# Kernel tuning notes

Hardware: AMD Instinct MI355X
Metric: run time of the kernel (lower is better)

The kernel has to match this reference:

```python
import math
import jax, jax.numpy as jnp
import numpy as np

# ---- static configuration (matches init_kwargs) ----
BATCH, F_IN, F_OUT = 8, 64, 128
B_IN, B_OUT = 32, 16
NL = B_OUT                    # spherical degrees l = 0..NL-1
MDIM = 2 * NL - 1             # dense order axis, m in [-(NL-1), NL-1]
N_BETA_G, N_ALPHA_G = 4, 8
MAX_BETA = math.pi / 8
N_GRID = N_BETA_G * N_ALPHA_G
SCALING = 1.0 / math.sqrt(N_GRID * F_IN * B_OUT ** 4.0 / B_IN ** 2.0)

_LF = np.concatenate([[0.0], np.cumsum(np.log(np.arange(1, 200, dtype=np.float64)))])  # log n!

def _wigner_d(l, betas):
    """Wigner small-d d^l_{m1,m2}(beta) -> [len(betas), 2l+1, 2l+1]."""
    m1 = np.arange(-l, l + 1).reshape(-1, 1, 1)
    m2 = np.arange(-l, l + 1).reshape(1, -1, 1)
    k = np.arange(0, 2 * l + 1).reshape(1, 1, -1)
    a1, a3, a4 = l + m2 - k, m1 - m2 + k, l - m1 - k
    valid = (a1 >= 0) & (a3 >= 0) & (a4 >= 0)
    logc = (0.5 * (_LF[l + m1] + _LF[l - m1] + _LF[l + m2] + _LF[l - m2])
            - _LF[np.clip(a1, 0, None)] - _LF[k]
            - _LF[np.clip(a3, 0, None)] - _LF[np.clip(a4, 0, None)])
    coef = np.where(valid, ((-1.0) ** (m1 - m2 + k)) * np.exp(logc), 0.0)
    c = np.cos(betas / 2.0)[:, None, None, None]
    s = np.sin(betas / 2.0)[:, None, None, None]
    ce = np.clip(2 * l + m2 - m1 - 2 * k, 0, None)
    se = np.clip(m1 - m2 + 2 * k, 0, None)
    return (coef[None] * (c ** ce) * (s ** se)).sum(-1)

# SOFT beta sampling grids
_betas_in = np.pi * (2 * np.arange(2 * B_IN) + 0.5) / (4 * B_IN)
_betas_out = np.pi * (2 * np.arange(2 * B_OUT) + 0.5) / (4 * B_OUT)

# Driscoll-Healy quadrature weights on the input beta grid (alpha measure 2pi/(2b) folded in)
_kk = np.arange(B_IN)
_w = ((2.0 * np.pi / (2 * B_IN)) * (2.0 / B_IN) * np.sin(_betas_in)
      * (np.sin(_betas_in[:, None] * (2 * _kk + 1)) / (2 * _kk + 1)).sum(1))

# kernel grid: s2_near_identity_grid(max_beta=pi/8, n_alpha=8, n_beta=4), beta-major order
_gb = MAX_BETA * np.arange(1, N_BETA_G + 1) / N_BETA_G
_ga = 2 * np.pi * np.arange(N_ALPHA_G) / N_ALPHA_G
GRID_BETA, GRID_ALPHA = [a.ravel() for a in np.meshgrid(_gb, _ga, indexing='ij')]

# W_ANA[beta_j, l, m]  = w_j * d^l_{m,0}(beta_j)            (S2 analysis)
# D_SYN[l, beta_k, m, n] = (2l+1) * d^l_{m,n}(beta_k)       (SO3 synthesis)
# FK[g, l, m]          = d^l_{m,0}(beta_g) * e^{i m alpha_g} (kernel real-FT, s2_rft)
W_ANA = np.zeros((2 * B_IN, NL, MDIM), np.float32)
D_SYN = np.zeros((NL, 2 * B_OUT, MDIM, MDIM), np.float32)
FK = np.zeros((N_GRID, NL, MDIM), np.complex64)
for l in range(NL):
    sl = slice(NL - 1 - l, NL + l)  # dense slots for m = -l..l
    W_ANA[:, l, sl] = (_w[:, None] * _wigner_d(l, _betas_in)[:, :, l]).astype(np.float32)
    D_SYN[l, :, sl, sl] = ((2 * l + 1) * _wigner_d(l, _betas_out)).astype(np.float32)
    m = np.arange(-l, l + 1)
    FK[:, l, sl] = (_wigner_d(l, GRID_BETA)[:, :, l]
                    * np.exp(1j * m[None, :] * GRID_ALPHA[:, None])).astype(np.complex64)
W_ANA, D_SYN, FK = jnp.asarray(W_ANA), jnp.asarray(D_SYN), jnp.asarray(FK)

_M_VALS = np.arange(-(NL - 1), NL)
_BINS_IN = _M_VALS % (2 * B_IN)  # fft bins of the alpha-frequencies m=-15..15


def setup_inputs() -> dict:
    key = jax.random.key(0)
    k1, k2 = jax.random.split(key)
    x = jax.random.normal(k1, (BATCH, F_IN, 2 * B_IN, 2 * B_IN), jnp.float32)
    kernel = jax.random.uniform(k2, (F_IN, F_OUT, N_GRID), jnp.float32, -1.0, 1.0)
    bias = jnp.zeros((1, F_OUT, 1, 1, 1), jnp.float32)
    return {"x": x, "kernel": kernel, "bias": bias}


def _s2_conv(x, kernel, bias):
    # ---- S2 FFT of the input: [B,Fin,2b_in(beta),2b_in(alpha)] -> spectrum [l,m,B,Fin] ----
    xf = jnp.fft.fft(x, axis=-1)              # e^{-i m alpha}
    xm = xf[..., _BINS_IN]                    # [B, Fin, 2b_in, MDIM]
    xhat = jnp.einsum('jlm,bfjm->lmbf', W_ANA, xm)            # [NL, MDIM, B, Fin] complex

    # ---- kernel spherical-harmonic expansion (s2_rft) ----
    kh = jnp.einsum('iog,glm->lmio', (kernel * SCALING).astype(jnp.complex64), FK)

    # ---- per-degree block matmul (s2_mm): z^l_{mn} = sum_i xhat^l_m[i] conj(kh^l_n[i]) ----
    z = jnp.einsum('lmbi,lnio->lmnbo', xhat, jnp.conj(kh))    # [NL, MDIM, MDIM, B, Fout]

    # ---- inverse SO(3) FFT: sum over degrees with (2l+1) d^l_{mn}(beta), then ifft2 over (alpha,gamma) ----
    fmn = jnp.einsum('lkmn,lmnbo->bokmn', D_SYN, z)           # [B, Fout, 2b_out, MDIM, MDIM]
    g = jnp.zeros((BATCH, F_OUT, 2 * B_OUT, 2 * B_OUT, 2 * B_OUT), fmn.dtype)
    g = g.at[..., :MDIM, :MDIM].set(fmn)
    g = jnp.roll(g, shift=(-(NL - 1), -(NL - 1)), axis=(-2, -1))  # m=0 at fft bin 0
    out = jnp.fft.ifft2(g, axes=(-2, -1)).real * float((2 * B_OUT) ** 2)  # e^{+i m alpha}
    return out.astype(jnp.float32) + bias


def reference(x, kernel, bias):
    return _s2_conv(x, kernel, bias)
```

## Files before the change

### kernel.cpp

```cpp
#include <hip/hip_runtime.h>
#include <stdint.h>
#include <math.h>


#define PI_D 3.14159265358979323846
#define SCALING_F 0.002762135864009951f

#define OFF_WANA 0
#define OFF_FKR  31744
#define OFF_FKI  47616
#define OFF_D3   63488
#define OFF_XHAT 317440
#define OFF_WT   317440
#define OFF_KHC  825344
#define OFF_Z2   3053568
#define OFF_T    11180032

typedef unsigned short u16t;
typedef __attribute__((ext_vector_type(8))) short s8v;
typedef __attribute__((ext_vector_type(8))) _Float16 h8v;
typedef __attribute__((ext_vector_type(4))) float f4v;

union frg { uint4 u; uint32_t w[4]; s8v s; h8v h; };

__device__ inline double ipow_d(double x, int e){
  double r = 1.0;
  while (e > 0){ if (e & 1) r *= x; x *= x; e >>= 1; }
  return r;
}

__device__ double wig_d(int l, int m1, int m2, double beta, const double* LF){
  double c = cos(0.5*beta), s = sin(0.5*beta);
  double sum = 0.0;
  for (int k = 0; k <= 2*l; ++k){
    int a1 = l + m2 - k, a3 = m1 - m2 + k, a4 = l - m1 - k;
    if (a1 < 0 || a3 < 0 || a4 < 0) continue;
    double logc = 0.5*(LF[l+m1]+LF[l-m1]+LF[l+m2]+LF[l-m2]) - LF[a1] - LF[k] - LF[a3] - LF[a4];
    double t = exp(logc) * ipow_d(c, a1 + a4) * ipow_d(s, a3 + k);
    sum += (a3 & 1) ? -t : t;
  }
  return sum;
}

__device__ inline uint32_t f2bf(float f){
  uint32_t u = __float_as_uint(f);
  return (u + 0x7fffu + ((u >> 16) & 1u)) >> 16;
}
__device__ inline float bf2f(uint32_t h){ return __uint_as_float((h & 0xffffu) << 16); }
__device__ inline float bf2f_lo(uint32_t h){ return __uint_as_float(h << 16); }
__device__ inline float bf2f_hi(uint32_t h){ return __uint_as_float(h & 0xffff0000u); }
__device__ inline uint32_t pack2(float a, float b){ return f2bf(a) | (f2bf(b) << 16); }

#define LF_INIT \
  __shared__ double LF[40]; \
  if (threadIdx.x == 0){ LF[0] = 0.0; double acc_ = 0.0; for (int n_ = 1; n_ < 40; ++n_){ acc_ += log((double)n_); LF[n_] = acc_; } } \
  __syncthreads();

__global__ void k_zero(float* __restrict__ ws){
  int id = blockIdx.x*256 + threadIdx.x;
  *reinterpret_cast<float4*>(ws + OFF_D3 + (size_t)id*4) = make_float4(0.f,0.f,0.f,0.f);
}

__global__ void k_consts(float* __restrict__ ws){
  LF_INIT
  int bid = blockIdx.x, tid = threadIdx.x;
  if (bid < 124){
    __shared__ double wj2[2];
    int id0 = bid*256;
    int jbase = id0/496;
    if (tid < 2){
      int j = jbase + tid;
      double wv_ = 0.0;
      if (j < 64){
        double beta = PI_D*(2*j + 0.5)/128.0;
        double wsum = 0.0;
        for (int kk = 0; kk < 32; ++kk) wsum += sin(beta*(2*kk+1))/(double)(2*kk+1);
        wv_ = (2.0*PI_D/64.0)*(2.0/32.0)*sin(beta)*wsum;
      }
      wj2[tid] = wv_;
    }
    __syncthreads();
    int id = id0 + tid;
    int m = id % 31, l = (id / 31) & 15, j = id / 496;
    int mp = m - 15, amp = mp < 0 ? -mp : mp;
    float val = 0.f;
    if (amp <= l){
      double beta = PI_D*(2*j + 0.5)/128.0;
      val = (float)(wj2[j - jbase] * wig_d(l, mp, 0, beta, LF));
    }
    ws[OFF_WANA + (l*31 + m)*64 + j] = val;
  } else if (bid < 186){
    int id = (bid - 124)*256 + tid;
    if (id >= 15872) return;
    int n = id % 31, l = (id / 31) & 15, g = id / 496;
    int np = n - 15, anp = np < 0 ? -np : np;
    float vr = 0.f, vi = 0.f;
    if (anp <= l){
      double beta = PI_D*((double)((g >> 3) + 1))/32.0;
      double alpha = (PI_D/4.0)*(double)(g & 7);
      double d = wig_d(l, np, 0, beta, LF);
      vr = (float)(d*cos(np*alpha));
      vi = (float)(d*sin(np*alpha));
    }
    ws[OFF_FKR + id] = vr;
    ws[OFF_FKI + id] = vi;
  } else if (bid < 698){
    int bb = bid - 186;
    int k = bb >> 4, l = bb & 15;
    int n21 = 2*l + 1, items = (l+1)*n21;
    double beta = PI_D*(2*k + 0.5)/64.0;
    float fl = (float)(2*l + 1);
    u16t* d3b = reinterpret_cast<u16t*>(ws + OFF_D3);
    for (int item = tid; item < items; item += 256){
      int im = item / n21, in = item - (item/n21)*n21;
      int mn = im*31 + in - l + 15;
      float v = fl * (float)wig_d(l, im, in - l, beta, LF);
      uint32_t hb = f2bf(v);
      uint32_t lb = f2bf(v - bf2f(hb));
      d3b[(mn*32 + k)*32 + l]      = (u16t)hb;
      d3b[(mn*32 + k)*32 + 16 + l] = (u16t)lb;
    }
  } else {
    u16t* wt = reinterpret_cast<u16t*>(ws + OFF_WT);
    for (int idx = tid; idx < 4096; idx += 256){
      int kidx = idx & 31, cc = (idx >> 5) & 15, h = (idx >> 9) & 1;
      int p = (idx >> 10) & 1, nt = (idx >> 11) & 1;
      int q = kidx & 1, nloc = kidx >> 1, n = h*16 + nloc, cg = nt*16 + cc;
      float val = 0.f;
      if (n <= 30){
        double th = 2.0*PI_D*(double)(((17 + n)*cg) & 31)/32.0;
        float wr = (float)cos(th), wi = (float)sin(th);
        val = p ? (q ? wr : wi) : (q ? -wi : wr);
      }
      union { _Float16 hh[2]; u16t us[2]; } cv;
      cv.hh[0] = (_Float16)val; cv.hh[1] = (_Float16)0.f;
      wt[idx] = cv.us[0];
    }
  }
}

__global__ void k_xhat(const float* __restrict__ x, float* __restrict__ ws){
  __shared__ float xl[4096];
  __shared__ float c64[64], s64[64];
  __shared__ float xmr[1024], xmi[1024];
  int tid = threadIdx.x;
  int b = blockIdx.x >> 6, i = blockIdx.x & 63;
  const float* xp = x + (b*64 + i)*4096;
  for (int idx = tid; idx < 4096; idx += 256) xl[idx] = xp[idx];
  if (tid < 64){ double a = 2.0*PI_D*tid/64.0; c64[tid] = (float)cos(a); s64[tid] = (float)sin(a); }
  __syncthreads();
  for (int item = tid; item < 1024; item += 256){
    int j = item >> 4, mi = item & 15;
    float re = 0.f, im = 0.f;
    const float* xr = xl + j*64;
    for (int a = 0; a < 64; ++a){
      int p = (mi*a) & 63;
      re += xr[a]*c64[p];
      im -= xr[a]*s64[p];
    }
    xmr[item] = re; xmi[item] = im;
  }
  __syncthreads();
  {
    int l = tid >> 4, mi = tid & 15;
    if (mi <= l){
      float rr = 0.f, ri = 0.f;
      const float* wrow = ws + OFF_WANA + (l*31 + 15 + mi)*64;
      for (int j = 0; j < 64; ++j){
        float w = wrow[j];
        rr += w * xmr[j*16 + mi];
        ri += w * xmi[j*16 + mi];
      }
      int dst = OFF_XHAT + ((l*31 + 15 + mi)*8 + b)*128 + i*2;
      ws[dst] = rr; ws[dst+1] = ri;
    }
  }
}

__global__ void k_khc(const float* __restrict__ kern, float* __restrict__ ws){
  __shared__ float kl2[32*66];
  __shared__ float fr[992], fi[992];
  int tid = threadIdx.x;
  int o = blockIdx.x >> 4, l = blockIdx.x & 15;
  for (int idx = tid; idx < 2048; idx += 256){
    int i = idx >> 5, g = idx & 31;
    kl2[g*66 + i] = kern[(i*128 + o)*32 + g];
  }
  for (int idx = tid; idx < 992; idx += 256){
    int g = idx / 31, n = idx - (idx/31)*31;
    fr[idx] = ws[OFF_FKR + g*496 + l*31 + n];
    fi[idx] = ws[OFF_FKI + g*496 + l*31 + n];
  }
  __syncthreads();
  uint32_t* khb = reinterpret_cast<uint32_t*>(ws + OFF_KHC);
  int c1 = (l*(l+1)) >> 1;
  int ntask = (l+1)*32;
  for (int t = tid; t < ntask; t += 256){
    int np = t >> 5, ip = t & 31, i0 = 2*ip;
    float ar0=0.f, ai0=0.f, ar1=0.f, ai1=0.f;
    for (int g = 0; g < 32; ++g){
      float2 kv = *reinterpret_cast<const float2*>(kl2 + g*66 + i0);
      float fv = fr[g*31 + 15 + np], gv = fi[g*31 + 15 + np];
      ar0 += kv.x*fv; ai0 -= kv.x*gv;
      ar1 += kv.y*fv; ai1 -= kv.y*gv;
    }
    size_t base = (size_t)((c1 + np)*128 + o)*64 + i0;
    khb[base]     = pack2(SCALING_F*ar0, SCALING_F*ai0);
    khb[base + 1] = pack2(SCALING_F*ar1, SCALING_F*ai1);
  }
}

__global__ __launch_bounds__(256) void k_zm(float* __restrict__ ws){
  __shared__ uint32_t lds_a[1024];
  __shared__ uint32_t lds_b[8192];
  int tid = threadIdx.x, lane = tid & 63, wv = tid >> 6;
  int c = lane & 15, g = lane >> 4;
  int bid = blockIdx.x;
  int b = bid / 136, t = bid - b*136;
  int l = (int)((sqrtf(8.f*(float)t + 1.f) - 1.f)*0.5f);
  while ((l+1)*(l+2)/2 <= t) ++l;
  while (l*(l+1)/2 > t) --l;
  int np = t - l*(l+1)/2;

  for (int idx = tid; idx < 1024; idx += 256){
    int m = idx >> 6, i = idx & 63;
    uint32_t v = 0u;
    if (m <= l){
      const float* xp = ws + OFF_XHAT + (((l*31 + 15 + m)*8 + b)*128 + 2*i);
      float2 xv = *reinterpret_cast<const float2*>(xp);
      v = pack2(xv.x, xv.y);
    }
    lds_a[(m*64 + i) ^ ((m & 7) << 2)] = v;
  }
  {
    const uint32_t* khb = reinterpret_cast<const uint32_t*>(ws + OFF_KHC);
    size_t rowbase = (size_t)((l*(l+1))/2 + np)*128;
    for (int idx4 = tid; idx4 < 2048; idx4 += 256){
      int o = idx4 >> 4, i4 = idx4 & 15;
      uint4 v = *reinterpret_cast<const uint4*>(khb + (rowbase + o)*64 + i4*4);
      *reinterpret_cast<uint4*>(lds_b + ((o*64 + i4*4) ^ ((o & 7) << 2))) = v;
    }
  }
  __syncthreads();

  frg af[4];
  #pragma unroll
  for (int tt = 0; tt < 4; ++tt)
    af[tt].u = *reinterpret_cast<const uint4*>(lds_a + ((c*64 + tt*16 + g*4) ^ ((c & 7) << 2)));

  uint32_t* z3 = reinterpret_cast<uint32_t*>(ws) + OFF_T;
  int rpos = l*l + l + np, rneg = l*l + l - np;
  for (int ot = wv; ot < 8; ot += 4){
    f4v arp = {0.f,0.f,0.f,0.f}, aip = {0.f,0.f,0.f,0.f};
    f4v arn = {0.f,0.f,0.f,0.f}, ain = {0.f,0.f,0.f,0.f};
    int oc = ot*16 + c;
    #pragma unroll
    for (int tt = 0; tt < 4; ++tt){
      frg bw;
      bw.u = *reinterpret_cast<const uint4*>(lds_b + ((oc*64 + tt*16 + g*4) ^ ((oc & 7) << 2)));
      frg brp, bip;
      #pragma unroll
      for (int j = 0; j < 4; ++j){
        uint32_t w = bw.w[j];
        uint32_t sw = (w >> 16) | (w << 16);
        brp.w[j] = w ^ 0x80000000u;
        bip.w[j] = sw;
      }
      arp = __builtin_amdgcn_mfma_f32_16x16x32_bf16(af[tt].s, brp.s, arp, 0, 0, 0);
      aip = __builtin_amdgcn_mfma_f32_16x16x32_bf16(af[tt].s, bip.s, aip, 0, 0, 0);
      if (np){
        frg brn, bin;
        #pragma unroll
        for (int j = 0; j < 4; ++j){
          uint32_t w = bw.w[j];
          uint32_t sw = (w >> 16) | (w << 16);
          if (np & 1){ brn.w[j] = w ^ 0x80008000u; bin.w[j] = sw ^ 0x80000000u; }
          else       { brn.w[j] = w;               bin.w[j] = sw ^ 0x00008000u; }
        }
        arn = __builtin_amdgcn_mfma_f32_16x16x32_bf16(af[tt].s, brn.s, arn, 0, 0, 0);
        ain = __builtin_amdgcn_mfma_f32_16x16x32_bf16(af[tt].s, bin.s, ain, 0, 0, 0);
      }
    }
    #pragma unroll
    for (int rr = 0; rr < 4; ++rr){
      int m = g*4 + rr;
      z3[((size_t)(b*256 + rpos)*16 + m)*128 + oc] = pack2(arp[rr], aip[rr]);
      if (np)
        z3[((size_t)(b*256 + rneg)*16 + m)*128 + oc] = pack2(arn[rr], ain[rr]);
    }
  }
}

__global__ __launch_bounds__(256) void k_tr(float* __restrict__ ws){
  __shared__ uint32_t zl[256*33];
  int tid = threadIdx.x, bid = blockIdx.x;
  int b = bid >> 6, m = (bid >> 2) & 15, h = bid & 3;
  const uint32_t* z3 = reinterpret_cast<const uint32_t*>(ws) + OFF_T;
  for (int idx = tid; idx < 8192; idx += 256){
    int r = idx >> 5, o = idx & 31;
    zl[r*33 + o] = z3[((size_t)(b*256 + r)*16 + m)*128 + h*32 + o];
  }
  __syncthreads();
  u16t* zr = reinterpret_cast<u16t*>(ws + OFF_Z2);
  u16t* zi = zr + 8126464;
  for (int task = tid; task < 992; task += 256){
    int nd = task >> 5, o = task & 31;
    int ndp = nd - 15, a = ndp < 0 ? -ndp : ndp;
    uint32_t re[8], im[8];
    #pragma unroll
    for (int j = 0; j < 8; ++j){
      uint32_t r0 = 0u, i0 = 0u, r1 = 0u, i1 = 0u;
      int l0 = 2*j, l1 = 2*j + 1;
      if (l0 >= a){ uint32_t v = zl[(l0*l0 + l0 + ndp)*33 + o]; r0 = v & 0xffffu; i0 = v >> 16; }
      if (l1 >= a){ uint32_t v = zl[(l1*l1 + l1 + ndp)*33 + o]; r1 = v & 0xffffu; i1 = v >> 16; }
      re[j] = r0 | (r1 << 16); im[j] = i0 | (i1 << 16);
    }
    size_t base = (size_t)(m*31 + nd)*16384 + (size_t)(b*128 + h*32 + o)*16;
    *reinterpret_cast<uint4*>(zr + base)     = make_uint4(re[0],re[1],re[2],re[3]);
    *reinterpret_cast<uint4*>(zr + base + 8) = make_uint4(re[4],re[5],re[6],re[7]);
    *reinterpret_cast<uint4*>(zi + base)     = make_uint4(im[0],im[1],im[2],im[3]);
    *reinterpret_cast<uint4*>(zi + base + 8) = make_uint4(im[4],im[5],im[6],im[7]);
  }
}

__global__ __launch_bounds__(512) void k_fmt(float* __restrict__ ws){
  __shared__ uint32_t fmb[16384];
  int tid = threadIdx.x;
  int lane = tid & 63, wv = tid >> 6;
  int c = lane & 15, g = lane >> 4;
  int bt = blockIdx.x >> 4, m = blockIdx.x & 15;
  const u16t* z2r = reinterpret_cast<const u16t*>(ws + OFF_Z2);
  const u16t* z2i = z2r + 8126464;
  const u16t* d3b = reinterpret_cast<const u16t*>(ws + OFF_D3);
  const u16t* wtb = reinterpret_cast<const u16t*>(ws + OFF_WT);
  fmb[31*512 + (tid ^ 16)] = 0u;

  frg wf[2][2][2];
  #pragma unroll
  for (int nt = 0; nt < 2; ++nt)
    #pragma unroll
    for (int p = 0; p < 2; ++p)
      #pragma unroll
      for (int h = 0; h < 2; ++h)
        wf[nt][p][h].u = *reinterpret_cast<const uint4*>(wtb + ((((nt*2+p)*2+h)*16 + c)*32 + g*8));

  {
    int l0 = (g & 1)*8;
    int hl16 = (g >> 1)*16;
    size_t bo16 = (size_t)(bt*16 + c)*16;
    #pragma unroll
    for (int t = 0; t < 4; ++t){
      int nd = wv*4 + t;
      if (nd > 30) break;
      int mn = m*31 + nd;
      frg ar, ai;
      ar.u = *reinterpret_cast<const uint4*>(z2r + (size_t)mn*16384 + bo16 + l0);
      ai.u = *reinterpret_cast<const uint4*>(z2i + (size_t)mn*16384 + bo16 + l0);
      int key = ((nd >> 2) & 1) << 4;
      #pragma unroll
      for (int kh = 0; kh < 2; ++kh){
        frg bf;
        bf.u = *reinterpret_cast<const uint4*>(d3b + ((size_t)mn*32 + kh*16 + c)*32 + hl16 + l0);
        f4v z4 = {0.f, 0.f, 0.f, 0.f};
        f4v cre = __builtin_amdgcn_mfma_f32_16x16x32_bf16(ar.s, bf.s, z4, 0, 0, 0);
        f4v cim = __builtin_amdgcn_mfma_f32_16x16x32_bf16(ai.s, bf.s, z4, 0, 0, 0);
        #pragma unroll
        for (int rr = 0; rr < 4; ++rr){
          int bok = (g*4 + rr)*32 + kh*16 + c;
          union { _Float16 hh[2]; uint32_t u; } pk;
          pk.hh[0] = (_Float16)cre[rr];
          pk.hh[1] = (_Float16)cim[rr];
          fmb[nd*512 + (bok ^ key)] = pk.u;
        }
      }
    }
  }
  __syncthreads();
  uint32_t* tglob = reinterpret_cast<uint32_t*>(ws) + OFF_T;
  #pragma unroll
  for (int q = 0; q < 4; ++q){
    int mt = wv*4 + q;
    int arow = mt*16 + c;
    frg A0, A1;
    #pragma unroll
    for (int j = 0; j < 4; ++j){
      int nd0 = g*4 + j, nd1 = nd0 + 16;
      A0.w[j] = fmb[nd0*512 + (arow ^ (((nd0 >> 2) & 1) << 4))];
      A1.w[j] = fmb[nd1*512 + (arow ^ (((nd1 >> 2) & 1) << 4))];
    }
    #pragma unroll
    for (int nt = 0; nt < 2; ++nt){
      f4v z4 = {0.f, 0.f, 0.f, 0.f};
      f4v tre = __builtin_amdgcn_mfma_f32_16x16x32_f16(A0.h, wf[nt][0][0].h, z4, 0, 0, 0);
      tre     = __builtin_amdgcn_mfma_f32_16x16x32_f16(A1.h, wf[nt][0][1].h, tre, 0, 0, 0);
      f4v tim = __builtin_amdgcn_mfma_f32_16x16x32_f16(A0.h, wf[nt][1][0].h, z4, 0, 0, 0);
      tim     = __builtin_amdgcn_mfma_f32_16x16x32_f16(A1.h, wf[nt][1][1].h, tim, 0, 0, 0);
      #pragma unroll
      for (int rr = 0; rr < 4; ++rr){
        int bokl = mt*16 + g*4 + rr;
        int bokg = (bt*16 + (bokl >> 5))*32 + (bokl & 31);
        tglob[(size_t)(bokg*16 + m)*32 + nt*16 + c] = pack2(tre[rr], tim[rr]);
      }
    }
  }
}

__global__ void k_out(const float* __restrict__ bias, float* __restrict__ out,
                      const float* __restrict__ ws){
  __shared__ uint32_t tl[2048];
  __shared__ float2 tw2[32];
  int tid = threadIdx.x;
  int b4 = blockIdx.x*4;
  const uint32_t* tg = reinterpret_cast<const uint32_t*>(ws) + OFF_T + (size_t)b4*512;
  for (int idx = tid; idx < 2048; idx += 256) tl[idx] = tg[idx];
  if (tid < 32){ double a = 2.0*PI_D*tid/32.0; tw2[tid] = make_float2((float)cos(a), (float)sin(a)); }
  __syncthreads();
  int aq = tid >> 5, c = tid & 31;
  for (int q = 0; q < 4; ++q){
    int bok = b4 + q;
    const uint32_t* tq = tl + q*512;
    float t0r = bf2f(tq[c]);
    float U0=0,U1=0,U2=0,U3=0,V0=0,V1=0,V2=0,V3=0;
    int p = aq;
    #pragma unroll
    for (int m = 1; m < 16; ++m){
      uint32_t wv = tq[m*32 + c];
      float tr = bf2f_lo(wv), ti = bf2f_hi(wv);
      float2 T = tw2[p];
      float u = tr*T.x - ti*T.y;
      float v = tr*T.y + ti*T.x;
      int j = m & 3;
      if      (j == 0){ U0 += u; V0 += v; }
      else if (j == 1){ U1 += u; V1 += v; }
      else if (j == 2){ U2 += u; V2 += v; }
      else            { U3 += u; V3 += v; }
      p = (p + aq) & 31;
    }
    float bia = bias[(bok >> 5) & 127];
    float* op = out + (size_t)bok*1024 + c;
    op[aq*32]      = t0r + 2.f*(U0+U1+U2+U3) + bia;
    op[(aq+8)*32]  = t0r + 2.f*(U0-V1-U2+V3) + bia;
    op[(aq+16)*32] = t0r + 2.f*(U0-U1+U2-U3) + bia;
    op[(aq+24)*32] = t0r + 2.f*(U0+V1-U2-V3) + bia;
  }
}

extern "C" void kernel_launch(void* const* d_in, const int* in_sizes, int n_in,
                              void* d_out, int out_size, void* d_ws, size_t ws_size,
                              hipStream_t stream) {
  const float* x    = (const float*)d_in[0];
  const float* kern = (const float*)d_in[1];
  const float* bias = (const float*)d_in[2];
  float* out = (float*)d_out;
  float* ws  = (float*)d_ws;

  k_zero  <<<dim3(248),  dim3(256), 0, stream>>>(ws);
  k_consts<<<dim3(699),  dim3(256), 0, stream>>>(ws);
  k_xhat  <<<dim3(512),  dim3(256), 0, stream>>>(x, ws);
  k_khc   <<<dim3(2048), dim3(256), 0, stream>>>(kern, ws);
  k_zm    <<<dim3(1088), dim3(256), 0, stream>>>(ws);
  k_tr    <<<dim3(512),  dim3(256), 0, stream>>>(ws);
  k_fmt   <<<dim3(1024), dim3(512), 0, stream>>>(ws);
  k_out   <<<dim3(8192), dim3(256), 0, stream>>>(bias, out, ws);
}
```

Baseline: 263.4 us.

## Fuse per-degree block matmul with transpose into one double-buffered kernel

Merges the z matmul kernel and the transpose kernel into a single kernel indexed by (batch, order n, half of degree range). Each block loops over degrees, double-buffering the kernel-coefficient and xhat tiles in LDS with register prefetch, accumulates results in a swizzled LDS output tile, and writes the final Z2 layout directly. This removes the intermediate z3 global round trip and one launch, but the negative-order products now reuse the same B tile without pairing, so the B loads are duplicated across positive and negative order blocks. Fewer, larger blocks (496) may reduce occupancy.

```diff
diff --git a/kernel.cpp b/kernel.cpp
--- a/kernel.cpp
+++ b/kernel.cpp
@@ -210,116 +210,123 @@
   }
 }
 
-__global__ __launch_bounds__(256) void k_zm(float* __restrict__ ws){
-  __shared__ uint32_t lds_a[1024];
-  __shared__ uint32_t lds_b[8192];
+__device__ inline int zswz(int o){ return (o ^ (o >> 3)) & 7; }
+
+__global__ __launch_bounds__(512) void k_zmt(float* __restrict__ ws){
+  __shared__ uint32_t lb[2][9216];
+  __shared__ uint32_t zout[16384];
   int tid = threadIdx.x, lane = tid & 63, wv = tid >> 6;
   int c = lane & 15, g = lane >> 4;
   int bid = blockIdx.x;
-  int b = bid / 136, t = bid - b*136;
-  int l = (int)((sqrtf(8.f*(float)t + 1.f) - 1.f)*0.5f);
-  while ((l+1)*(l+2)/2 <= t) ++l;
-  while (l*(l+1)/2 > t) --l;
-  int np = t - l*(l+1)/2;
-
-  for (int idx = tid; idx < 1024; idx += 256){
-    int m = idx >> 6, i = idx & 63;
-    uint32_t v = 0u;
-    if (m <= l){
-      const float* xp = ws + OFF_XHAT + (((l*31 + 15 + m)*8 + b)*128 + 2*i);
-      float2 xv = *reinterpret_cast<const float2*>(xp);
-      v = pack2(xv.x, xv.y);
-    }
-    lds_a[(m*64 + i) ^ ((m & 7) << 2)] = v;
-  }
-  {
-    const uint32_t* khb = reinterpret_cast<const uint32_t*>(ws + OFF_KHC);
-    size_t rowbase = (size_t)((l*(l+1))/2 + np)*128;
-    for (int idx4 = tid; idx4 < 2048; idx4 += 256){
+  int b = bid / 62, t = bid - b*62;
+  int nd = t >> 1, h = t & 1;
+  int ndp = nd - 15, a = ndp < 0 ? -ndp : ndp;
+  int neg = ndp < 0;
+  int l_lo = a > 8*h ? a : 8*h;
+  int l_hi = 8*h + 7;
+
+  for (int i = tid; i < 16384; i += 512) zout[i] = 0u;
+
+  const uint32_t* khb = reinterpret_cast<const uint32_t*>(ws + OFF_KHC);
+
+  if (l_lo <= l_hi){
+    size_t rowb = (size_t)((l_lo*(l_lo+1))/2 + a)*128;
+    #pragma unroll
+    for (int t4 = 0; t4 < 4; ++t4){
+      int idx4 = t4*512 + tid;
       int o = idx4 >> 4, i4 = idx4 & 15;
-      uint4 v = *reinterpret_cast<const uint4*>(khb + (rowbase + o)*64 + i4*4);
-      *reinterpret_cast<uint4*>(lds_b + ((o*64 + i4*4) ^ ((o & 7) << 2))) = v;
-    }
-  }
-  __syncthreads();
-
-  frg af[4];
-  #pragma unroll
-  for (int tt = 0; tt < 4; ++tt)
-    af[tt].u = *reinterpret_cast<const uint4*>(lds_a + ((c*64 + tt*16 + g*4) ^ ((c & 7) << 2)));
-
-  uint32_t* z3 = reinterpret_cast<uint32_t*>(ws) + OFF_T;
-  int rpos = l*l + l + np, rneg = l*l + l - np;
-  for (int ot = wv; ot < 8; ot += 4){
-    f4v arp = {0.f,0.f,0.f,0.f}, aip = {0.f,0.f,0.f,0.f};
-    f4v arn = {0.f,0.f,0.f,0.f}, ain = {0.f,0.f,0.f,0.f};
-    int oc = ot*16 + c;
+      uint4 v = *reinterpret_cast<const uint4*>(khb + (rowb + o)*64 + i4*4);
+      *reinterpret_cast<uint4*>(lb[0] + ((o*64 + i4*4) ^ ((o & 7) << 2))) = v;
+    }
+    int m = tid >> 5, i0 = (tid & 31)*2;
+    uint32_t a0 = 0u, a1 = 0u;
+    if (m <= l_lo){
+      float4 xv = *reinterpret_cast<const float4*>(ws + OFF_XHAT + (((l_lo*31 + 15 + m)*8 + b)*128 + i0*2));
+      a0 = pack2(xv.x, xv.y); a1 = pack2(xv.z, xv.w);
+    }
+    int ai_ = (m*64 + i0) ^ ((m & 7) << 2);
+    lb[0][8192 + ai_] = a0; lb[0][8192 + ai_ + 1] = a1;
+  }
+  __syncthreads();
+
+  int cur = 0;
+  for (int l = l_lo; l <= l_hi; ++l){
+    uint4 pB[4]; float4 pA = make_float4(0.f,0.f,0.f,0.f);
+    int pm = tid >> 5, pi0 = (tid & 31)*2;
+    bool pf = (l < l_hi);
+    if (pf){
+      int lx = l + 1;
+      size_t rowb = (size_t)((lx*(lx+1))/2 + a)*128;
+      #pragma unroll
+      for (int t4 = 0; t4 < 4; ++t4){
+        int idx4 = t4*512 + tid;
+        int o = idx4 >> 4, i4 = idx4 & 15;
+        pB[t4] = *reinterpret_cast<const uint4*>(khb + (rowb + o)*64 + i4*4);
+      }
+      if (pm <= lx)
+        pA = *reinterpret_cast<const float4*>(ws + OFF_XHAT + (((lx*31 + 15 + pm)*8 + b)*128 + pi0*2));
+    }
+    uint32_t* B = lb[cur];
+    uint32_t* A = lb[cur] + 8192;
+    frg af[4];
+    #pragma unroll
+    for (int tt = 0; tt < 4; ++tt)
+      af[tt].u = *reinterpret_cast<const uint4*>(A + ((c*64 + tt*16 + g*4) ^ ((c & 7) << 2)));
+    int oc = wv*16 + c;
+    f4v ar = {0.f,0.f,0.f,0.f}, ai = {0.f,0.f,0.f,0.f};
     #pragma unroll
     for (int tt = 0; tt < 4; ++tt){
       frg bw;
-      bw.u = *reinterpret_cast<const uint4*>(lds_b + ((oc*64 + tt*16 + g*4) ^ ((oc & 7) << 2)));
-      frg brp, bip;
+      bw.u = *reinterpret_cast<const uint4*>(B + ((oc*64 + tt*16 + g*4) ^ ((oc & 7) << 2)));
+      frg br_, bi_;
       #pragma unroll
       for (int j = 0; j < 4; ++j){
         uint32_t w = bw.w[j];
         uint32_t sw = (w >> 16) | (w << 16);
-        brp.w[j] = w ^ 0x80000000u;
-        bip.w[j] = sw;
-      }
-      arp = __builtin_amdgcn_mfma_f32_16x16x32_bf16(af[tt].s, brp.s, arp, 0, 0, 0);
-      aip = __builtin_amdgcn_mfma_f32_16x16x32_bf16(af[tt].s, bip.s, aip, 0, 0, 0);
-      if (np){
-        frg brn, bin;
-        #pragma unroll
-        for (int j = 0; j < 4; ++j){
-          uint32_t w = bw.w[j];
-          uint32_t sw = (w >> 16) | (w << 16);
-          if (np & 1){ brn.w[j] = w ^ 0x80008000u; bin.w[j] = sw ^ 0x80000000u; }
-          else       { brn.w[j] = w;               bin.w[j] = sw ^ 0x00008000u; }
-        }
-        arn = __builtin_amdgcn_mfma_f32_16x16x32_bf16(af[tt].s, brn.s, arn, 0, 0, 0);
-        ain = __builtin_amdgcn_mfma_f32_16x16x32_bf16(af[tt].s, bin.s, ain, 0, 0, 0);
-      }
-    }
+        if (!neg){ br_.w[j] = w ^ 0x80000000u; bi_.w[j] = sw; }
+        else if (a & 1){ br_.w[j] = w ^ 0x80008000u; bi_.w[j] = sw ^ 0x80000000u; }
+        else { br_.w[j] = w; bi_.w[j] = sw ^ 0x00008000u; }
+      }
+      ar = __builtin_amdgcn_mfma_f32_16x16x32_bf16(af[tt].s, br_.s, ar, 0, 0, 0);
+      ai = __builtin_amdgcn_mfma_f32_16x16x32_bf16(af[tt].s, bi_.s, ai, 0, 0, 0);
+    }
+    int lq = l - 8*h;
     #pragma unroll
     for (int rr = 0; rr < 4; ++rr){
       int m = g*4 + rr;
-      z3[((size_t)(b*256 + rpos)*16 + m)*128 + oc] = pack2(arp[rr], aip[rr]);
-      if (np)
-        z3[((size_t)(b*256 + rneg)*16 + m)*128 + oc] = pack2(arn[rr], ain[rr]);
-    }
-  }
-}
-
-__global__ __launch_bounds__(256) void k_tr(float* __restrict__ ws){
-  __shared__ uint32_t zl[256*33];
-  int tid = threadIdx.x, bid = blockIdx.x;
-  int b = bid >> 6, m = (bid >> 2) & 15, h = bid & 3;
-  const uint32_t* z3 = reinterpret_cast<const uint32_t*>(ws) + OFF_T;
-  for (int idx = tid; idx < 8192; idx += 256){
-    int r = idx >> 5, o = idx & 31;
-    zl[r*33 + o] = z3[((size_t)(b*256 + r)*16 + m)*128 + h*32 + o];
-  }
-  __syncthreads();
+      zout[(m*128 + oc)*8 + (lq ^ zswz(oc))] = pack2(ar[rr], ai[rr]);
+    }
+    if (pf){
+      uint32_t* D = lb[cur ^ 1];
+      #pragma unroll
+      for (int t4 = 0; t4 < 4; ++t4){
+        int idx4 = t4*512 + tid;
+        int o = idx4 >> 4, i4 = idx4 & 15;
+        *reinterpret_cast<uint4*>(D + ((o*64 + i4*4) ^ ((o & 7) << 2))) = pB[t4];
+      }
+      int ai_ = (pm*64 + pi0) ^ ((pm & 7) << 2);
+      uint32_t a0 = 0u, a1 = 0u;
+      if (pm <= l + 1){ a0 = pack2(pA.x, pA.y); a1 = pack2(pA.z, pA.w); }
+      D[8192 + ai_] = a0; D[8192 + ai_ + 1] = a1;
+    }
+    __syncthreads();
+    cur ^= 1;
+  }
+
   u16t* zr = reinterpret_cast<u16t*>(ws + OFF_Z2);
   u16t* zi = zr + 8126464;
-  for (int task = tid; task < 992; task += 256){
-    int nd = task >> 5, o = task & 31;
-    int ndp = nd - 15, a = ndp < 0 ? -ndp : ndp;
-    uint32_t re[8], im[8];
-    #pragma unroll
-    for (int j = 0; j < 8; ++j){
-      uint32_t r0 = 0u, i0 = 0u, r1 = 0u, i1 = 0u;
-      int l0 = 2*j, l1 = 2*j + 1;
-      if (l0 >= a){ uint32_t v = zl[(l0*l0 + l0 + ndp)*33 + o]; r0 = v & 0xffffu; i0 = v >> 16; }
-      if (l1 >= a){ uint32_t v = zl[(l1*l1 + l1 + ndp)*33 + o]; r1 = v & 0xffffu; i1 = v >> 16; }
-      re[j] = r0 | (r1 << 16); im[j] = i0 | (i1 << 16);
-    }
-    size_t base = (size_t)(m*31 + nd)*16384 + (size_t)(b*128 + h*32 + o)*16;
-    *reinterpret_cast<uint4*>(zr + base)     = make_uint4(re[0],re[1],re[2],re[3]);
-    *reinterpret_cast<uint4*>(zr + base + 8) = make_uint4(re[4],re[5],re[6],re[7]);
-    *reinterpret_cast<uint4*>(zi + base)     = make_uint4(im[0],im[1],im[2],im[3]);
-    *reinterpret_cast<uint4*>(zi + base + 8) = make_uint4(im[4],im[5],im[6],im[7]);
+  for (int idx = tid; idx < 2048; idx += 512){
+    int m = idx >> 7, o = idx & 127;
+    uint32_t v[8];
+    #pragma unroll
+    for (int lq = 0; lq < 8; ++lq) v[lq] = zout[(m*128 + o)*8 + (lq ^ zswz(o))];
+    uint4 reQ = make_uint4((v[0]&0xffffu)|(v[1]<<16), (v[2]&0xffffu)|(v[3]<<16),
+                           (v[4]&0xffffu)|(v[5]<<16), (v[6]&0xffffu)|(v[7]<<16));
+    uint4 imQ = make_uint4((v[0]>>16)|(v[1]&0xffff0000u), (v[2]>>16)|(v[3]&0xffff0000u),
+                           (v[4]>>16)|(v[5]&0xffff0000u), (v[6]>>16)|(v[7]&0xffff0000u));
+    size_t base = (size_t)(m*31 + nd)*16384 + (size_t)(b*128 + o)*16 + h*8;
+    *reinterpret_cast<uint4*>(zr + base) = reQ;
+    *reinterpret_cast<uint4*>(zi + base) = imQ;
   }
 }
 
@@ -458,8 +465,7 @@
   k_consts<<<dim3(699),  dim3(256), 0, stream>>>(ws);
   k_xhat  <<<dim3(512),  dim3(256), 0, stream>>>(x, ws);
   k_khc   <<<dim3(2048), dim3(256), 0, stream>>>(kern, ws);
-  k_zm    <<<dim3(1088), dim3(256), 0, stream>>>(ws);
-  k_tr    <<<dim3(512),  dim3(256), 0, stream>>>(ws);
+  k_zmt   <<<dim3(496),  dim3(512), 0, stream>>>(ws);
   k_fmt   <<<dim3(1024), dim3(512), 0, stream>>>(ws);
   k_out   <<<dim3(8192), dim3(256), 0, stream>>>(bias, out, ws);
 }
```

Result: slower. 298.2 us (+13.2%).
